# Kernel tuning notes

Measured on AMD Instinct MI355X. Metric: run time of the kernel, lower is better.

The kernel has to match this reference:

```python
import jax, jax.numpy as jnp
import numpy as np

K = 3          # kernel_size
STRIDE_H = 1
STRIDE_W = 1


def setup_inputs() -> dict:
    key = jax.random.key(0)
    k1, k2, k3, k4 = jax.random.split(key, 4)
    inputs = jax.random.normal(k1, (8, 128, 128, 128), dtype=jnp.float32)
    weight = jax.random.normal(k2, (128, 128, K, K), dtype=jnp.float32) * 0.05
    # learned per-image rate map, fractional dilations in [1, 3)
    rates = jax.random.uniform(k3, (1, 1, 32, 32), dtype=jnp.float32) * 2.0 + 1.0
    bias = jax.random.normal(k4, (128,), dtype=jnp.float32) * 0.01
    return {"inputs": inputs, "weight": weight, "rates": rates, "bias": bias}


def _interp_bilinear(r, out_h, out_w):
    # torch F.interpolate(mode='bilinear', align_corners=False) on a 2D map r[in_h,in_w]
    in_h, in_w = r.shape
    def src(n_out, n_in):
        s = (jnp.arange(n_out, dtype=jnp.float32) + 0.5) * (n_in / n_out) - 0.5
        return jnp.clip(s, 0.0, n_in - 1.0)
    sy = src(out_h, in_h)
    sx = src(out_w, in_w)
    y0 = jnp.floor(sy).astype(jnp.int32)
    x0 = jnp.floor(sx).astype(jnp.int32)
    y1 = jnp.minimum(y0 + 1, in_h - 1)
    x1 = jnp.minimum(x0 + 1, in_w - 1)
    wy = (sy - y0.astype(jnp.float32))[:, None]   # [out_h,1]
    wx = (sx - x0.astype(jnp.float32))[None, :]   # [1,out_w]
    return (r[y0[:, None], x0[None, :]] * (1 - wy) * (1 - wx)
            + r[y0[:, None], x1[None, :]] * (1 - wy) * wx
            + r[y1[:, None], x0[None, :]] * wy * (1 - wx)
            + r[y1[:, None], x1[None, :]] * wy * wx)


def _bilinear_sample(img, y, x):
    # img: [N,C,H,W]; y,x: [Ho,Wo] float positions; zero padding outside.
    H, W = img.shape[2], img.shape[3]
    y0 = jnp.floor(y).astype(jnp.int32)
    x0 = jnp.floor(x).astype(jnp.int32)
    y1, x1 = y0 + 1, x0 + 1
    wy = y - y0.astype(img.dtype)
    wx = x - x0.astype(img.dtype)
    def tap(yi, xi):
        m = ((yi >= 0) & (yi < H) & (xi >= 0) & (xi < W)).astype(img.dtype)
        yc = jnp.clip(yi, 0, H - 1)
        xc = jnp.clip(xi, 0, W - 1)
        return img[:, :, yc, xc] * m  # [N,C,Ho,Wo]
    return (tap(y0, x0) * (1 - wy) * (1 - wx)
            + tap(y0, x1) * (1 - wy) * wx
            + tap(y1, x0) * wy * (1 - wx)
            + tap(y1, x1) * wy * wx)


def reference(inputs, weight, rates, bias):
    N, Cin, H, W = inputs.shape
    Ho = (H - K) // STRIDE_H + 1
    Wo = (W - K) // STRIDE_W + 1
    rate = _interp_bilinear(rates[0, 0], Ho, Wo)          # [Ho,Wo]
    base_y = jnp.arange(Ho, dtype=jnp.float32)[:, None] * STRIDE_H
    base_x = jnp.arange(Wo, dtype=jnp.float32)[None, :] * STRIDE_W
    out = jnp.broadcast_to(bias[None, :, None, None], (N, weight.shape[0], Ho, Wo)).astype(inputs.dtype)
    # fixed K*K = 9 taps; each tap samples the input at p0 + k*rate (per-pixel dilation)
    for kh in range(K):
        for kw in range(K):
            y = base_y + kh * rate
            x = base_x + kw * rate
            samp = _bilinear_sample(inputs, y, x)          # [N,Cin,Ho,Wo]
            out = out + jnp.einsum('oc,nchw->nohw', weight[:, :, kh, kw], samp)
    return out
```

## Files before the change

kernel.cpp:

```cpp
#include <hip/hip_runtime.h>
#include <hip/hip_fp16.h>

#define N_    8
#define CIN   128
#define COUT  128
#define H_    128
#define W_    128
#define HO    126
#define WO    126
#define PIXPER (HO*WO)
#define TOTPIX (N_*PIXPER)
#define PT    128
#define BLKPERIMG 125
#define NBLK  (N_*BLKPERIMG)
#define SSTR  136

typedef _Float16 f16x8 __attribute__((ext_vector_type(8)));
typedef _Float16 f16x4 __attribute__((ext_vector_type(4)));
typedef float    f32x4 __attribute__((ext_vector_type(4)));

union U4H {
    uint4   u;
    __half2 h[4];
    f16x8   f;
};

__global__ __launch_bounds__(256) void transpose_in_kernel(
    const float* __restrict__ in, _Float16* __restrict__ in_cl)
{
    __shared__ float tile[64][65];
    int bid = blockIdx.x;
    int hwt = bid & 255;
    int ct  = (bid >> 8) & 1;
    int n   = bid >> 9;
    int r0  = threadIdx.x >> 4;
    int c4  = (threadIdx.x & 15) * 4;
    const float* src = in + ((size_t)(n * CIN + ct * 64) * 16384) + hwt * 64;
#pragma unroll
    for (int k = 0; k < 4; ++k) {
        int row = r0 + k * 16;
        float4 v = *(const float4*)(src + (size_t)row * 16384 + c4);
        *(float4*)&tile[row][c4] = v;
    }
    __syncthreads();
    _Float16* dst = in_cl + ((size_t)(n * 16384 + hwt * 64) * 128) + ct * 64;
#pragma unroll
    for (int k = 0; k < 4; ++k) {
        int hw = r0 + k * 16;
        f16x4 o;
        o[0] = (_Float16)tile[c4 + 0][hw];
        o[1] = (_Float16)tile[c4 + 1][hw];
        o[2] = (_Float16)tile[c4 + 2][hw];
        o[3] = (_Float16)tile[c4 + 3][hw];
        *(f16x4*)(dst + (size_t)hw * 128 + c4) = o;
    }
}

__global__ void transpose_w_kernel(const float* __restrict__ w, _Float16* __restrict__ wt) {
    int t = blockIdx.x * 256 + threadIdx.x;
    int o = t >> 7, c = t & 127;
    const float* s = w + (size_t)(o * 128 + c) * 9;
#pragma unroll
    for (int tap = 0; tap < 9; ++tap)
        wt[tap * 16384 + o * 128 + c] = (_Float16)s[tap];
}

__global__ __launch_bounds__(256, 2) void adc_main(
    const _Float16* __restrict__ in_cl, const _Float16* __restrict__ wt,
    const float* __restrict__ rates, const float* __restrict__ bias,
    float* __restrict__ out)
{
    __shared__ uint4    sW[2048];
    __shared__ __align__(16) _Float16 sS[PT * SSTR];
    __shared__ int      sPYi[3][PT];
    __shared__ float    sPYf[3][PT];
    __shared__ int      sPXi[3][PT];
    __shared__ float    sPXf[3][PT];

    const int t    = threadIdx.x;
    const int lane = t & 63;
    const int wv   = t >> 6;
    const int l15  = lane & 15;
    const int quad = lane >> 4;

    const int n     = blockIdx.x & 7;
    const int pbase = (blockIdx.x >> 3) * PT;

    if (t < PT) {
        int rem = min(pbase + t, PIXPER - 1);
        int ho = rem / WO, wo = rem - ho * WO;
        const float sc = 32.0f / 126.0f;
        float sy = fminf(fmaxf(((float)ho + 0.5f) * sc - 0.5f, 0.0f), 31.0f);
        float sx = fminf(fmaxf(((float)wo + 0.5f) * sc - 0.5f, 0.0f), 31.0f);
        int y0 = (int)sy, x0 = (int)sx;
        int y1 = min(y0 + 1, 31), x1 = min(x0 + 1, 31);
        float wy = sy - (float)y0, wx = sx - (float)x0;
        float r = rates[y0 * 32 + x0] * (1.0f - wy) * (1.0f - wx)
                + rates[y0 * 32 + x1] * (1.0f - wy) * wx
                + rates[y1 * 32 + x0] * wy * (1.0f - wx)
                + rates[y1 * 32 + x1] * wy * wx;
#pragma unroll
        for (int k = 0; k < 3; ++k) {
            float fy  = (float)ho + (float)k * r;
            float fy0 = floorf(fy);
            sPYi[k][t] = (int)fy0;
            sPYf[k][t] = fy - fy0;
            float fx  = (float)wo + (float)k * r;
            float fx0 = floorf(fx);
            sPXi[k][t] = (int)fx0;
            sPXf[k][t] = fx - fx0;
        }
    }

    f32x4 acc[8][2];
    const f32x4 zero = {0.0f, 0.0f, 0.0f, 0.0f};
#pragma unroll
    for (int i = 0; i < 8; ++i) { acc[i][0] = zero; acc[i][1] = zero; }

    __syncthreads();

    const int grp = t >> 4;
    const int gl  = t & 15;
    const unsigned nbase = (unsigned)n << 14;

#pragma unroll
    for (int tap = 0; tap < 9; ++tap) {
        const int kh = tap / 3;
        const int kw = tap - kh * 3;

        const uint4* wsrc = (const uint4*)(wt + tap * 16384);
#pragma unroll
        for (int i = 0; i < 8; ++i) {
            int gi = i * 256 + t;
            int o = gi >> 4, g = gi & 15;
            sW[(o << 4) | (g ^ (o & 7))] = wsrc[gi];
        }

#pragma unroll
        for (int j = 0; j < 8; ++j) {
            int px = grp * 8 + j;
            int   y0 = sPYi[kh][px];  float wy = sPYf[kh][px];
            int   x0 = sPXi[kw][px];  float wx = sPXf[kw][px];
            int yc0 = min(y0, H_ - 1), yc1 = min(y0 + 1, H_ - 1);
            int xc0 = min(x0, W_ - 1), xc1 = min(x0 + 1, W_ - 1);
            unsigned lo = (unsigned)(gl * 8);
            U4H A, B, C, D, S;
            A.u = *(const uint4*)(in_cl + (((nbase + (unsigned)(yc0 * W_ + xc0)) << 7) + lo));
            if (kw != 0) B.u = *(const uint4*)(in_cl + (((nbase + (unsigned)(yc0 * W_ + xc1)) << 7) + lo));
            if (kh != 0) C.u = *(const uint4*)(in_cl + (((nbase + (unsigned)(yc1 * W_ + xc0)) << 7) + lo));
            if (kh != 0 && kw != 0)
                         D.u = *(const uint4*)(in_cl + (((nbase + (unsigned)(yc1 * W_ + xc1)) << 7) + lo));
            if (kh == 0 && kw == 0) {
                S.u = A.u;
            } else {
                float vy0 = (y0 <= H_ - 1) ? 1.0f : 0.0f;
                float vy1 = (y0 <= H_ - 2) ? 1.0f : 0.0f;
                float vx0 = (x0 <= W_ - 1) ? 1.0f : 0.0f;
                float vx1 = (x0 <= W_ - 2) ? 1.0f : 0.0f;
                __half2 w00v = __float2half2_rn((1.0f - wy) * (1.0f - wx) * vy0 * vx0);
                __half2 w01v = __float2half2_rn((1.0f - wy) * wx * vy0 * vx1);
                __half2 w10v = __float2half2_rn(wy * (1.0f - wx) * vy1 * vx0);
                __half2 w11v = __float2half2_rn(wy * wx * vy1 * vx1);
#pragma unroll
                for (int d = 0; d < 4; ++d) {
                    __half2 s = __hmul2(A.h[d], w00v);
                    if (kw != 0)            s = __hfma2(B.h[d], w01v, s);
                    if (kh != 0)            s = __hfma2(C.h[d], w10v, s);
                    if (kh != 0 && kw != 0) s = __hfma2(D.h[d], w11v, s);
                    S.h[d] = s;
                }
            }
            *(f16x8*)&sS[px * SSTR + gl * 8] = S.f;
        }
        __syncthreads();

#pragma unroll
        for (int ks = 0; ks < 4; ++ks) {
            f16x8 b0 = *(const f16x8*)&sS[(wv * 32 +      l15) * SSTR + ks * 32 + quad * 8];
            f16x8 b1 = *(const f16x8*)&sS[(wv * 32 + 16 + l15) * SSTR + ks * 32 + quad * 8];
#pragma unroll
            for (int mt = 0; mt < 8; ++mt) {
                int o = (mt << 4) | l15;
                int g = (ks << 2) | quad;
                U4H AF;
                AF.u = sW[(o << 4) | (g ^ (o & 7))];
                acc[mt][0] = __builtin_amdgcn_mfma_f32_16x16x32_f16(AF.f, b0, acc[mt][0], 0, 0, 0);
                acc[mt][1] = __builtin_amdgcn_mfma_f32_16x16x32_f16(AF.f, b1, acc[mt][1], 0, 0, 0);
            }
        }
        __syncthreads();
    }

#pragma unroll
    for (int pt = 0; pt < 2; ++pt) {
        int p    = (wv << 5) + (pt << 4) + l15;
        int prel = pbase + p;
        int rem2 = min(prel, PIXPER - 1);
        float* obase = out + (size_t)n * (COUT * PIXPER) + rem2;
        if (prel < PIXPER) {
#pragma unroll
            for (int mt = 0; mt < 8; ++mt) {
                int o0 = (mt << 4) + (quad << 2);
                float4 bs = *(const float4*)(bias + o0);
                f32x4 a0 = acc[mt][pt];
                obase[(size_t)(o0 + 0) * PIXPER] = a0[0] + bs.x;
                obase[(size_t)(o0 + 1) * PIXPER] = a0[1] + bs.y;
                obase[(size_t)(o0 + 2) * PIXPER] = a0[2] + bs.z;
                obase[(size_t)(o0 + 3) * PIXPER] = a0[3] + bs.w;
            }
        }
    }
}

extern "C" void kernel_launch(void* const* d_in, const int* in_sizes, int n_in,
                              void* d_out, int out_size, void* d_ws, size_t ws_size,
                              hipStream_t stream) {
    const float* inputs = (const float*)d_in[0];
    const float* weight = (const float*)d_in[1];
    const float* rates  = (const float*)d_in[2];
    const float* bias   = (const float*)d_in[3];
    float* out = (float*)d_out;

    char* ws = (char*)d_ws;
    _Float16* in_cl = (_Float16*)ws;
    _Float16* wtp   = (_Float16*)(ws + 33554432);

    transpose_w_kernel<<<64, 256, 0, stream>>>(weight, wtp);
    transpose_in_kernel<<<4096, 256, 0, stream>>>(inputs, in_cl);
    adc_main<<<NBLK, 256, 0, stream>>>(in_cl, wtp, rates, bias, out);
}
```

Before: 189.8 us.

## Gather bilinear samples directly into MFMA B-fragments, drop sample LDS staging

Each lane now computes the sample coordinates for its own MFMA B-operand pixels and builds the interpolated fp16 fragments in registers. This removes the shared-memory sample tile, the per-tap coordinate tables and one barrier per tap. LDS use falls to the weight tile only, and the launch bound asks for 4 blocks per CU to raise occupancy. In exchange, each lane recomputes coordinates per tap, issues narrower 16-byte gathers spread over four channel groups instead of one coalesced row, and may run short of registers at the higher occupancy target.

Measured after the change: 286.8 us. 1.51x slower.

```diff
diff --git a/kernel.cpp b/kernel.cpp
--- a/kernel.cpp
+++ b/kernel.cpp
@@ -13,7 +13,6 @@
 #define PT    128
 #define BLKPERIMG 125
 #define NBLK  (N_*BLKPERIMG)
-#define SSTR  136
 
 typedef _Float16 f16x8 __attribute__((ext_vector_type(8)));
 typedef _Float16 f16x4 __attribute__((ext_vector_type(4)));
@@ -65,17 +64,12 @@
         wt[tap * 16384 + o * 128 + c] = (_Float16)s[tap];
 }
 
-__global__ __launch_bounds__(256, 2) void adc_main(
+__global__ __launch_bounds__(256, 4) void adc_main(
     const _Float16* __restrict__ in_cl, const _Float16* __restrict__ wt,
     const float* __restrict__ rates, const float* __restrict__ bias,
     float* __restrict__ out)
 {
-    __shared__ uint4    sW[2048];
-    __shared__ __align__(16) _Float16 sS[PT * SSTR];
-    __shared__ int      sPYi[3][PT];
-    __shared__ float    sPYf[3][PT];
-    __shared__ int      sPXi[3][PT];
-    __shared__ float    sPXf[3][PT];
+    __shared__ uint4 sW[2048];
 
     const int t    = threadIdx.x;
     const int lane = t & 63;
@@ -85,31 +79,25 @@
 
     const int n     = blockIdx.x & 7;
     const int pbase = (blockIdx.x >> 3) * PT;
-
-    if (t < PT) {
-        int rem = min(pbase + t, PIXPER - 1);
-        int ho = rem / WO, wo = rem - ho * WO;
+    const unsigned nbase = (unsigned)n << 14;
+
+    int   hoA[2], woA[2];
+    float rA[2];
+#pragma unroll
+    for (int h = 0; h < 2; ++h) {
+        int pc = min(pbase + (wv << 5) + (h << 4) + l15, PIXPER - 1);
+        int ho = pc / WO, wo = pc - ho * WO;
+        hoA[h] = ho; woA[h] = wo;
         const float sc = 32.0f / 126.0f;
         float sy = fminf(fmaxf(((float)ho + 0.5f) * sc - 0.5f, 0.0f), 31.0f);
         float sx = fminf(fmaxf(((float)wo + 0.5f) * sc - 0.5f, 0.0f), 31.0f);
         int y0 = (int)sy, x0 = (int)sx;
         int y1 = min(y0 + 1, 31), x1 = min(x0 + 1, 31);
         float wy = sy - (float)y0, wx = sx - (float)x0;
-        float r = rates[y0 * 32 + x0] * (1.0f - wy) * (1.0f - wx)
-                + rates[y0 * 32 + x1] * (1.0f - wy) * wx
-                + rates[y1 * 32 + x0] * wy * (1.0f - wx)
-                + rates[y1 * 32 + x1] * wy * wx;
-#pragma unroll
-        for (int k = 0; k < 3; ++k) {
-            float fy  = (float)ho + (float)k * r;
-            float fy0 = floorf(fy);
-            sPYi[k][t] = (int)fy0;
-            sPYf[k][t] = fy - fy0;
-            float fx  = (float)wo + (float)k * r;
-            float fx0 = floorf(fx);
-            sPXi[k][t] = (int)fx0;
-            sPXf[k][t] = fx - fx0;
-        }
+        rA[h] = rates[y0 * 32 + x0] * (1.0f - wy) * (1.0f - wx)
+              + rates[y0 * 32 + x1] * (1.0f - wy) * wx
+              + rates[y1 * 32 + x0] * wy * (1.0f - wx)
+              + rates[y1 * 32 + x1] * wy * wx;
     }
 
     f32x4 acc[8][2];
@@ -117,17 +105,73 @@
 #pragma unroll
     for (int i = 0; i < 8; ++i) { acc[i][0] = zero; acc[i][1] = zero; }
 
-    __syncthreads();
-
-    const int grp = t >> 4;
-    const int gl  = t & 15;
-    const unsigned nbase = (unsigned)n << 14;
+    const unsigned co = (unsigned)(quad << 3);
 
 #pragma unroll
     for (int tap = 0; tap < 9; ++tap) {
         const int kh = tap / 3;
         const int kw = tap - kh * 3;
 
+        f16x8 bf[2][4];
+#pragma unroll
+        for (int h = 0; h < 2; ++h) {
+            const int   ho = hoA[h], wo = woA[h];
+            const float r  = rA[h];
+            int y0, x0; float wy, wx;
+            if (kh == 0) { y0 = ho; wy = 0.0f; }
+            else {
+                float fy = (float)ho + (float)kh * r;
+                float f0 = floorf(fy); y0 = (int)f0; wy = fy - f0;
+            }
+            if (kw == 0) { x0 = wo; wx = 0.0f; }
+            else {
+                float fx = (float)wo + (float)kw * r;
+                float f0 = floorf(fx); x0 = (int)f0; wx = fx - f0;
+            }
+            const int yc0 = min(y0, H_ - 1), yc1 = min(y0 + 1, H_ - 1);
+            const int xc0 = min(x0, W_ - 1), xc1 = min(x0 + 1, W_ - 1);
+            const unsigned a00 = ((nbase + (unsigned)(yc0 * W_ + xc0)) << 7) + co;
+            const unsigned a01 = ((nbase + (unsigned)(yc0 * W_ + xc1)) << 7) + co;
+            const unsigned a10 = ((nbase + (unsigned)(yc1 * W_ + xc0)) << 7) + co;
+            const unsigned a11 = ((nbase + (unsigned)(yc1 * W_ + xc1)) << 7) + co;
+
+            if (kh == 0 && kw == 0) {
+#pragma unroll
+                for (int ks = 0; ks < 4; ++ks) {
+                    U4H A; A.u = *(const uint4*)(in_cl + a00 + ks * 32);
+                    bf[h][ks] = A.f;
+                }
+            } else {
+                const float vy0 = (y0 <= H_ - 1) ? 1.0f : 0.0f;
+                const float vy1 = (y0 <= H_ - 2) ? 1.0f : 0.0f;
+                const float vx0 = (x0 <= W_ - 1) ? 1.0f : 0.0f;
+                const float vx1 = (x0 <= W_ - 2) ? 1.0f : 0.0f;
+                const __half2 w00v = __float2half2_rn((1.0f - wy) * (1.0f - wx) * vy0 * vx0);
+                const __half2 w01v = __float2half2_rn((1.0f - wy) * wx * vy0 * vx1);
+                const __half2 w10v = __float2half2_rn(wy * (1.0f - wx) * vy1 * vx0);
+                const __half2 w11v = __float2half2_rn(wy * wx * vy1 * vx1);
+#pragma unroll
+                for (int ks = 0; ks < 4; ++ks) {
+                    U4H A, B, C, D, S;
+                    A.u = *(const uint4*)(in_cl + a00 + ks * 32);
+                    if (kw != 0) B.u = *(const uint4*)(in_cl + a01 + ks * 32);
+                    if (kh != 0) C.u = *(const uint4*)(in_cl + a10 + ks * 32);
+                    if (kh != 0 && kw != 0)
+                                 D.u = *(const uint4*)(in_cl + a11 + ks * 32);
+#pragma unroll
+                    for (int d = 0; d < 4; ++d) {
+                        __half2 s = __hmul2(A.h[d], w00v);
+                        if (kw != 0)            s = __hfma2(B.h[d], w01v, s);
+                        if (kh != 0)            s = __hfma2(C.h[d], w10v, s);
+                        if (kh != 0 && kw != 0) s = __hfma2(D.h[d], w11v, s);
+                        S.h[d] = s;
+                    }
+                    bf[h][ks] = S.f;
+                }
+            }
+        }
+
+        __syncthreads();
         const uint4* wsrc = (const uint4*)(wt + tap * 16384);
 #pragma unroll
         for (int i = 0; i < 8; ++i) {
@@ -135,60 +179,20 @@
             int o = gi >> 4, g = gi & 15;
             sW[(o << 4) | (g ^ (o & 7))] = wsrc[gi];
         }
-
-#pragma unroll
-        for (int j = 0; j < 8; ++j) {
-            int px = grp * 8 + j;
-            int   y0 = sPYi[kh][px];  float wy = sPYf[kh][px];
-            int   x0 = sPXi[kw][px];  float wx = sPXf[kw][px];
-            int yc0 = min(y0, H_ - 1), yc1 = min(y0 + 1, H_ - 1);
-            int xc0 = min(x0, W_ - 1), xc1 = min(x0 + 1, W_ - 1);
-            unsigned lo = (unsigned)(gl * 8);
-            U4H A, B, C, D, S;
-            A.u = *(const uint4*)(in_cl + (((nbase + (unsigned)(yc0 * W_ + xc0)) << 7) + lo));
-            if (kw != 0) B.u = *(const uint4*)(in_cl + (((nbase + (unsigned)(yc0 * W_ + xc1)) << 7) + lo));
-            if (kh != 0) C.u = *(const uint4*)(in_cl + (((nbase + (unsigned)(yc1 * W_ + xc0)) << 7) + lo));
-            if (kh != 0 && kw != 0)
-                         D.u = *(const uint4*)(in_cl + (((nbase + (unsigned)(yc1 * W_ + xc1)) << 7) + lo));
-            if (kh == 0 && kw == 0) {
-                S.u = A.u;
-            } else {
-                float vy0 = (y0 <= H_ - 1) ? 1.0f : 0.0f;
-                float vy1 = (y0 <= H_ - 2) ? 1.0f : 0.0f;
-                float vx0 = (x0 <= W_ - 1) ? 1.0f : 0.0f;
-                float vx1 = (x0 <= W_ - 2) ? 1.0f : 0.0f;
-                __half2 w00v = __float2half2_rn((1.0f - wy) * (1.0f - wx) * vy0 * vx0);
-                __half2 w01v = __float2half2_rn((1.0f - wy) * wx * vy0 * vx1);
-                __half2 w10v = __float2half2_rn(wy * (1.0f - wx) * vy1 * vx0);
-                __half2 w11v = __float2half2_rn(wy * wx * vy1 * vx1);
-#pragma unroll
-                for (int d = 0; d < 4; ++d) {
-                    __half2 s = __hmul2(A.h[d], w00v);
-                    if (kw != 0)            s = __hfma2(B.h[d], w01v, s);
-                    if (kh != 0)            s = __hfma2(C.h[d], w10v, s);
-                    if (kh != 0 && kw != 0) s = __hfma2(D.h[d], w11v, s);
-                    S.h[d] = s;
-                }
-            }
-            *(f16x8*)&sS[px * SSTR + gl * 8] = S.f;
-        }
         __syncthreads();
 
 #pragma unroll
         for (int ks = 0; ks < 4; ++ks) {
-            f16x8 b0 = *(const f16x8*)&sS[(wv * 32 +      l15) * SSTR + ks * 32 + quad * 8];
-            f16x8 b1 = *(const f16x8*)&sS[(wv * 32 + 16 + l15) * SSTR + ks * 32 + quad * 8];
 #pragma unroll
             for (int mt = 0; mt < 8; ++mt) {
                 int o = (mt << 4) | l15;
                 int g = (ks << 2) | quad;
                 U4H AF;
                 AF.u = sW[(o << 4) | (g ^ (o & 7))];
-                acc[mt][0] = __builtin_amdgcn_mfma_f32_16x16x32_f16(AF.f, b0, acc[mt][0], 0, 0, 0);
-                acc[mt][1] = __builtin_amdgcn_mfma_f32_16x16x32_f16(AF.f, b1, acc[mt][1], 0, 0, 0);
-            }
-        }
-        __syncthreads();
+                acc[mt][0] = __builtin_amdgcn_mfma_f32_16x16x32_f16(AF.f, bf[0][ks], acc[mt][0], 0, 0, 0);
+                acc[mt][1] = __builtin_amdgcn_mfma_f32_16x16x32_f16(AF.f, bf[1][ks], acc[mt][1], 0, 0, 0);
+            }
+        }
     }
 
 #pragma unroll
```

## Prefetch next tap's gathers across MFMA phase and load weights via global_load_lds

Applied to the files above, without the earlier changes.

The per-tap input gathers are split into two half-batches held in registers, and the first half for the next tap is issued before the MFMA loop so its global latency overlaps with compute. Weight tiles are pre-swizzled in the transpose kernel and copied straight into LDS with global_load_lds, which avoids a register round trip. The sampled tile drops its padded stride in favour of an XOR swizzle to avoid bank conflicts. The register-held gather buffer raises VGPR pressure and could reduce occupancy under the two-blocks launch bound.

After: 186.3 us. Within noise of the previous version (-1.9%).

```diff
diff --git a/kernel.cpp b/kernel.cpp
--- a/kernel.cpp
+++ b/kernel.cpp
@@ -13,7 +13,6 @@
 #define PT    128
 #define BLKPERIMG 125
 #define NBLK  (N_*BLKPERIMG)
-#define SSTR  136
 
 typedef _Float16 f16x8 __attribute__((ext_vector_type(8)));
 typedef _Float16 f16x4 __attribute__((ext_vector_type(4)));
@@ -24,6 +23,10 @@
     __half2 h[4];
     f16x8   f;
 };
+
+#define GLLDS(gp, lp) __builtin_amdgcn_global_load_lds( \
+    (const __attribute__((address_space(1))) unsigned int*)(gp), \
+    (__attribute__((address_space(3))) unsigned int*)(lp), 16, 0, 0)
 
 __global__ __launch_bounds__(256) void transpose_in_kernel(
     const float* __restrict__ in, _Float16* __restrict__ in_cl)
@@ -59,10 +62,72 @@
 __global__ void transpose_w_kernel(const float* __restrict__ w, _Float16* __restrict__ wt) {
     int t = blockIdx.x * 256 + threadIdx.x;
     int o = t >> 7, c = t & 127;
+    int g = c >> 3;
+    int dst = (((o << 4) | (g ^ (o & 7))) << 3) | (c & 7);
     const float* s = w + (size_t)(o * 128 + c) * 9;
 #pragma unroll
     for (int tap = 0; tap < 9; ++tap)
-        wt[tap * 16384 + o * 128 + c] = (_Float16)s[tap];
+        wt[tap * 16384 + dst] = (_Float16)s[tap];
+}
+
+__device__ __forceinline__ void gather_issue(
+    int KH, int KW, U4H (&G)[4][4], int j0, int grp, int gl, unsigned nbase,
+    const _Float16* __restrict__ in_cl,
+    const int (*sPYi)[PT], const int (*sPXi)[PT])
+{
+    const unsigned lo = (unsigned)(gl * 8);
+#pragma unroll
+    for (int jj = 0; jj < 4; ++jj) {
+        int px = grp * 8 + j0 + jj;
+        int y0 = sPYi[KH][px];
+        int x0 = sPXi[KW][px];
+        int yc0 = min(y0, H_ - 1), yc1 = min(y0 + 1, H_ - 1);
+        int xc0 = min(x0, W_ - 1), xc1 = min(x0 + 1, W_ - 1);
+        G[jj][0].u = *(const uint4*)(in_cl + (((nbase + (unsigned)(yc0 * W_ + xc0)) << 7) + lo));
+        if (KW != 0)
+            G[jj][1].u = *(const uint4*)(in_cl + (((nbase + (unsigned)(yc0 * W_ + xc1)) << 7) + lo));
+        if (KH != 0)
+            G[jj][2].u = *(const uint4*)(in_cl + (((nbase + (unsigned)(yc1 * W_ + xc0)) << 7) + lo));
+        if (KH != 0 && KW != 0)
+            G[jj][3].u = *(const uint4*)(in_cl + (((nbase + (unsigned)(yc1 * W_ + xc1)) << 7) + lo));
+    }
+}
+
+__device__ __forceinline__ void gather_lerp_store(
+    int KH, int KW, U4H (&G)[4][4], int j0, int grp, int gl,
+    _Float16* sS,
+    const int (*sPYi)[PT], const float (*sPYf)[PT],
+    const int (*sPXi)[PT], const float (*sPXf)[PT])
+{
+#pragma unroll
+    for (int jj = 0; jj < 4; ++jj) {
+        int j  = j0 + jj;
+        int px = grp * 8 + j;
+        U4H S;
+        if (KH == 0 && KW == 0) {
+            S = G[jj][0];
+        } else {
+            int   y0 = sPYi[KH][px];  float wy = sPYf[KH][px];
+            int   x0 = sPXi[KW][px];  float wx = sPXf[KW][px];
+            float vy0 = (y0 <= H_ - 1) ? 1.0f : 0.0f;
+            float vy1 = (y0 <= H_ - 2) ? 1.0f : 0.0f;
+            float vx0 = (x0 <= W_ - 1) ? 1.0f : 0.0f;
+            float vx1 = (x0 <= W_ - 2) ? 1.0f : 0.0f;
+            __half2 w00 = __float2half2_rn((1.0f - wy) * (1.0f - wx) * vy0 * vx0);
+            __half2 w01 = __float2half2_rn((1.0f - wy) * wx * vy0 * vx1);
+            __half2 w10 = __float2half2_rn(wy * (1.0f - wx) * vy1 * vx0);
+            __half2 w11 = __float2half2_rn(wy * wx * vy1 * vx1);
+#pragma unroll
+            for (int d = 0; d < 4; ++d) {
+                __half2 s = __hmul2(G[jj][0].h[d], w00);
+                if (KW != 0)              s = __hfma2(G[jj][1].h[d], w01, s);
+                if (KH != 0)              s = __hfma2(G[jj][2].h[d], w10, s);
+                if (KH != 0 && KW != 0)   s = __hfma2(G[jj][3].h[d], w11, s);
+                S.h[d] = s;
+            }
+        }
+        *(f16x8*)&sS[px * 128 + ((unsigned)(gl ^ j)) * 8] = S.f;
+    }
 }
 
 __global__ __launch_bounds__(256, 2) void adc_main(
@@ -71,7 +136,7 @@
     float* __restrict__ out)
 {
     __shared__ uint4    sW[2048];
-    __shared__ __align__(16) _Float16 sS[PT * SSTR];
+    __shared__ __align__(16) _Float16 sS[PT * 128];
     __shared__ int      sPYi[3][PT];
     __shared__ float    sPYf[3][PT];
     __shared__ int      sPXi[3][PT];
@@ -85,6 +150,7 @@
 
     const int n     = blockIdx.x & 7;
     const int pbase = (blockIdx.x >> 3) * PT;
+    const unsigned nbase = (unsigned)n << 14;
 
     if (t < PT) {
         int rem = min(pbase + t, PIXPER - 1);
@@ -117,11 +183,14 @@
 #pragma unroll
     for (int i = 0; i < 8; ++i) { acc[i][0] = zero; acc[i][1] = zero; }
 
-    __syncthreads();
-
     const int grp = t >> 4;
     const int gl  = t & 15;
-    const unsigned nbase = (unsigned)n << 14;
+
+    __syncthreads();
+
+    U4H G[4][4];
+
+    gather_issue(0, 0, G, 0, grp, gl, nbase, in_cl, sPYi, sPXi);
 
 #pragma unroll
     for (int tap = 0; tap < 9; ++tap) {
@@ -131,59 +200,34 @@
         const uint4* wsrc = (const uint4*)(wt + tap * 16384);
 #pragma unroll
         for (int i = 0; i < 8; ++i) {
-            int gi = i * 256 + t;
-            int o = gi >> 4, g = gi & 15;
-            sW[(o << 4) | (g ^ (o & 7))] = wsrc[gi];
-        }
-
-#pragma unroll
-        for (int j = 0; j < 8; ++j) {
-            int px = grp * 8 + j;
-            int   y0 = sPYi[kh][px];  float wy = sPYf[kh][px];
-            int   x0 = sPXi[kw][px];  float wx = sPXf[kw][px];
-            int yc0 = min(y0, H_ - 1), yc1 = min(y0 + 1, H_ - 1);
-            int xc0 = min(x0, W_ - 1), xc1 = min(x0 + 1, W_ - 1);
-            unsigned lo = (unsigned)(gl * 8);
-            U4H A, B, C, D, S;
-            A.u = *(const uint4*)(in_cl + (((nbase + (unsigned)(yc0 * W_ + xc0)) << 7) + lo));
-            if (kw != 0) B.u = *(const uint4*)(in_cl + (((nbase + (unsigned)(yc0 * W_ + xc1)) << 7) + lo));
-            if (kh != 0) C.u = *(const uint4*)(in_cl + (((nbase + (unsigned)(yc1 * W_ + xc0)) << 7) + lo));
-            if (kh != 0 && kw != 0)
-                         D.u = *(const uint4*)(in_cl + (((nbase + (unsigned)(yc1 * W_ + xc1)) << 7) + lo));
-            if (kh == 0 && kw == 0) {
-                S.u = A.u;
-            } else {
-                float vy0 = (y0 <= H_ - 1) ? 1.0f : 0.0f;
-                float vy1 = (y0 <= H_ - 2) ? 1.0f : 0.0f;
-                float vx0 = (x0 <= W_ - 1) ? 1.0f : 0.0f;
-                float vx1 = (x0 <= W_ - 2) ? 1.0f : 0.0f;
-                __half2 w00v = __float2half2_rn((1.0f - wy) * (1.0f - wx) * vy0 * vx0);
-                __half2 w01v = __float2half2_rn((1.0f - wy) * wx * vy0 * vx1);
-                __half2 w10v = __float2half2_rn(wy * (1.0f - wx) * vy1 * vx0);
-                __half2 w11v = __float2half2_rn(wy * wx * vy1 * vx1);
-#pragma unroll
-                for (int d = 0; d < 4; ++d) {
-                    __half2 s = __hmul2(A.h[d], w00v);
-                    if (kw != 0)            s = __hfma2(B.h[d], w01v, s);
-                    if (kh != 0)            s = __hfma2(C.h[d], w10v, s);
-                    if (kh != 0 && kw != 0) s = __hfma2(D.h[d], w11v, s);
-                    S.h[d] = s;
-                }
-            }
-            *(f16x8*)&sS[px * SSTR + gl * 8] = S.f;
-        }
+            int base = i * 256 + (wv << 6);
+            GLLDS(wsrc + base + lane, &sW[base]);
+        }
+
+        gather_lerp_store(kh, kw, G, 0, grp, gl, sS, sPYi, sPYf, sPXi, sPXf);
+        gather_issue(kh, kw, G, 4, grp, gl, nbase, in_cl, sPYi, sPXi);
+        gather_lerp_store(kh, kw, G, 4, grp, gl, sS, sPYi, sPYf, sPXi, sPXf);
+
         __syncthreads();
 
+        if (tap < 8) {
+            const int tap1 = tap + 1;
+            const int kh1 = tap1 / 3;
+            const int kw1 = tap1 - kh1 * 3;
+            gather_issue(kh1, kw1, G, 0, grp, gl, nbase, in_cl, sPYi, sPXi);
+        }
+
 #pragma unroll
         for (int ks = 0; ks < 4; ++ks) {
-            f16x8 b0 = *(const f16x8*)&sS[(wv * 32 +      l15) * SSTR + ks * 32 + quad * 8];
-            f16x8 b1 = *(const f16x8*)&sS[(wv * 32 + 16 + l15) * SSTR + ks * 32 + quad * 8];
+            const int g  = (ks << 2) | quad;
+            const int sw = g ^ (l15 & 7);
+            f16x8 b0 = *(const f16x8*)&sS[(wv * 32 +      l15) * 128 + sw * 8];
+            f16x8 b1 = *(const f16x8*)&sS[(wv * 32 + 16 + l15) * 128 + sw * 8];
 #pragma unroll
             for (int mt = 0; mt < 8; ++mt) {
                 int o = (mt << 4) | l15;
-                int g = (ks << 2) | quad;
                 U4H AF;
-                AF.u = sW[(o << 4) | (g ^ (o & 7))];
+                AF.u = sW[(o << 4) | sw];
                 acc[mt][0] = __builtin_amdgcn_mfma_f32_16x16x32_f16(AF.f, b0, acc[mt][0], 0, 0, 0);
                 acc[mt][1] = __builtin_amdgcn_mfma_f32_16x16x32_f16(AF.f, b1, acc[mt][1], 0, 0, 0);
             }
```
